# Kernel tuning notes

Measured on AMD Instinct MI355X. Metric: run time of the kernel, lower is better.

The kernel has to match this reference:

```python
import jax, jax.numpy as jnp
import numpy as np
from jax import lax

B, NR, NT, M, NUM_ITER = 16384, 64, 32, 4, 64


def setup_inputs() -> dict:
    key = jax.random.key(0)
    k1, k2, k3 = jax.random.split(key, 3)
    yt = jax.random.normal(k1, (B, NR), dtype=jnp.float32)
    # scale channel to keep the 64-step unrolled descent numerically stable
    Ht = 0.1 * jax.random.normal(k2, (B, NR, NT), dtype=jnp.float32)
    sigmat0 = 0.5 + 0.5 * jax.random.uniform(k3, (B,), dtype=jnp.float32)
    m = jnp.array([-3.0, -1.0, 1.0, 3.0], dtype=jnp.float32)          # 4-PAM constellation
    alpha = jnp.full((M,), 0.25, dtype=jnp.float32)                    # uniform prior
    taui = jnp.ones((NUM_ITER + 1,), dtype=jnp.float32)                # taui0 = 1
    delta = jnp.full((NUM_ITER,), 0.1, dtype=jnp.float32)              # delta0 = 0.1
    return {"yt": yt, "Ht": Ht, "sigmat0": sigmat0, "m": m, "alpha": alpha,
            "taui": taui, "delta": delta}


def reference(yt, Ht, sigmat0, m, alpha, taui, delta):
    # Precompute as in CMDNet.call
    HH = jnp.einsum('bri,brj->bij', Ht, Ht)          # [B, Nt, Nt] = H^T H
    yH = jnp.einsum('br,brj->bj', yt, Ht)            # [B, Nt]     = y^T H
    Bsz, _, Nt = Ht.shape
    Mc = m.shape[0]
    n_iter = delta.shape[0]

    G0 = jnp.zeros((Bsz, Nt, Mc), dtype=Ht.dtype)
    sig2 = (sigmat0 ** 2)[:, None, None]             # [B,1,1]
    log_alpha = jnp.log(alpha)                       # [M]
    taui_abs = jnp.abs(taui)                         # [num_iter+1]
    # first layer uses scale 1 in the softmax (first_iter=True), but taui_abs in grad_x
    ft_scale = taui_abs[:n_iter].at[0].set(1.0)

    def step(G, inp):
        scale, ta, d = inp
        ft = jax.nn.softmax((log_alpha + G) * scale, axis=-1)   # [B,Nt,M]
        xt = jnp.sum(ft * m, axis=-1)                           # [B,Nt] soft symbol
        xHH = jnp.einsum('bi,bij->bj', xt, HH)                  # [B,Nt]
        grad_x = ta * (ft * m - ft * xt[..., None])             # [B,Nt,M]
        grad_L = sig2 * (1.0 - jnp.exp(-G)) + grad_x * (xHH - yH)[..., None]
        return G - d * grad_L, None

    G, _ = lax.scan(step, G0, (ft_scale, taui_abs[:n_iter], delta))

    # last layer (last_iter=True): softmax + soft symbol only, no update
    ft = jax.nn.softmax((log_alpha + G) * taui_abs[n_iter], axis=-1)
    xt = jnp.sum(ft * m, axis=-1)
    return ft, xt
```

## Files before the change

kernel.cpp:

```cpp
#include <hip/hip_runtime.h>


#define NRr 64
#define NTt 32
#define NITER 64
#define B_TOTAL 16384

using f16x8  = __attribute__((ext_vector_type(8))) _Float16;
using h16x2  = __attribute__((ext_vector_type(2))) _Float16;
using f32x16 = __attribute__((ext_vector_type(16))) float;

static __device__ __forceinline__ uint32_t pk16(float a, float b) {
    union { _Float16 h[2]; uint32_t u; } x;
    x.h[0] = (_Float16)a; x.h[1] = (_Float16)b;
    return x.u;
}

static __device__ __forceinline__ float fdot2u(uint32_t a, uint32_t b, float c) {
    union { uint32_t u; h16x2 h; } x, y;
    x.u = a; y.u = b;
#if __has_builtin(__builtin_amdgcn_fdot2)
    return __builtin_amdgcn_fdot2(x.h, y.h, c, false);
#else
    return c + (float)x.h[0] * (float)y.h[0] + (float)x.h[1] * (float)y.h[1];
#endif
}

static __device__ __forceinline__ float exp2fast(float x) {
#if __has_builtin(__builtin_amdgcn_exp2f)
    return __builtin_amdgcn_exp2f(x);
#else
    return exp2f(x);
#endif
}

static __device__ __forceinline__ float rdlane(float v, int lane) {
    return __builtin_bit_cast(float,
        __builtin_amdgcn_readlane(__builtin_bit_cast(int, v), lane));
}

static __device__ __forceinline__ float rfl(float v) {
    return __builtin_bit_cast(float,
        __builtin_amdgcn_readfirstlane(__builtin_bit_cast(int, v)));
}

static __device__ __forceinline__ void gram_one(
    const float* __restrict__ hp, const float* __restrict__ ypt,
    const int hi, uint32_t ap[8], float& ypart_out)
{
    f32x16 acc = {};
    float  ypart = 0.f;
#pragma unroll
    for (int kc = 0; kc < 4; ++kc) {
        const int kb = kc * 16 + hi * 8;
        float h[8];
#pragma unroll
        for (int e = 0; e < 8; ++e) h[e] = hp[(size_t)(kb + e) * NTt];
        const float4 ya = *(const float4*)(ypt + kb);
        const float4 yb = *(const float4*)(ypt + kb + 4);
        ypart += h[0]*ya.x + h[1]*ya.y + h[2]*ya.z + h[3]*ya.w
               + h[4]*yb.x + h[5]*yb.y + h[6]*yb.z + h[7]*yb.w;
        f16x8 fa;
#pragma unroll
        for (int e = 0; e < 8; ++e) fa[e] = (_Float16)h[e];
        acc = __builtin_amdgcn_mfma_f32_32x32x16_f16(fa, fa, acc, 0, 0, 0);
    }
#pragma unroll
    for (int g = 0; g < 4; ++g) {
        ap[2*g+0] = pk16(acc[4*g+0], acc[4*g+1]);
        ap[2*g+1] = pk16(acc[4*g+2], acc[4*g+3]);
    }
    ypart_out = ypart;
}

static __device__ __forceinline__ void exch_hh(
    const uint32_t apx[8], const uint32_t apy[8], const int hi, uint32_t hh[16])
{
#pragma unroll
    for (int p = 0; p < 8; ++p) {
        const uint32_t snd = hi ? apx[p] : apy[p];
        const uint32_t rcv = (uint32_t)__shfl_xor((int)snd, 32, 64);
        const uint32_t own = hi ? apy[p] : apx[p];
        const int g = p >> 1, cc = p & 1;
        hh[4*g + cc]     = hi ? rcv : own;
        hh[4*g + 2 + cc] = hi ? own : rcv;
    }
}

__global__ __launch_bounds__(256)
__attribute__((amdgpu_waves_per_eu(4, 4)))
void cmdnet_kernel(
    const float* __restrict__ yt,
    const float* __restrict__ Ht,
    const float* __restrict__ sig0,
    const float* __restrict__ mm,
    const float* __restrict__ alpha,
    const float* __restrict__ taui,
    const float* __restrict__ delta,
    float* __restrict__ out)
{
    __shared__ __align__(16) _Float16 xtsh[4][4][32];

    const int tid = threadIdx.x;
    const int w   = tid >> 6;
    const int l   = tid & 63;
    const int j   = l & 31;
    const int hi  = l >> 5;
    const int c0  = (blockIdx.x * 4 + w) * 4;

    const float vta = fabsf(taui[l]);
    const float vd  = delta[l];

    const size_t hstride = (size_t)NRr * NTt;

    uint32_t hhA[16], hhB[16];
    float yHA_v, yHB_v;
    {
        uint32_t apx[8], apy[8];
        float ypx, ypy;
        gram_one(Ht + (size_t)(c0    ) * hstride + j, yt + (size_t)(c0    ) * NRr, hi, apx, ypx);
        gram_one(Ht + (size_t)(c0 + 2) * hstride + j, yt + (size_t)(c0 + 2) * NRr, hi, apy, ypy);
        exch_hh(apx, apy, hi, hhA);
        const float snd = hi ? ypx : ypy;
        const float rcv = __shfl_xor(snd, 32, 64);
        yHA_v = (hi ? ypy : ypx) + rcv;
    }
    {
        uint32_t apx[8], apy[8];
        float ypx, ypy;
        gram_one(Ht + (size_t)(c0 + 1) * hstride + j, yt + (size_t)(c0 + 1) * NRr, hi, apx, ypx);
        gram_one(Ht + (size_t)(c0 + 3) * hstride + j, yt + (size_t)(c0 + 3) * NRr, hi, apy, ypy);
        exch_hh(apx, apy, hi, hhB);
        const float snd = hi ? ypx : ypy;
        const float rcv = __shfl_xor(snd, 32, 64);
        yHB_v = (hi ? ypy : ypx) + rcv;
    }

    const int bA = c0 + 2*hi;
    const int bB = bA + 1;
    const float sgA = sig0[bA], sgB = sig0[bB];
    const float sig2A = sgA * sgA, sig2B = sgB * sgB;

    const float4 mv = *(const float4*)mm;
    const float4 av = *(const float4*)alpha;
    const float m0 = rfl(mv.x), m1 = rfl(mv.y), m2 = rfl(mv.z), m3 = rfl(mv.w);
    const float la0 = rfl(__log2f(av.x)), la1 = rfl(__log2f(av.y));
    const float la2 = rfl(__log2f(av.z)), la3 = rfl(__log2f(av.w));

    const float L2E  = 1.4426950408889634f;
    const float NL2E = -1.4426950408889634f;

    _Float16* xwA = &xtsh[w][2*hi][j];
    _Float16* xwB = &xtsh[w][2*hi+1][j];
    const uint4* xr = (const uint4*)&xtsh[w][2*hi][0];

    float GA0 = 0.f, GA1 = 0.f, GA2 = 0.f, GA3 = 0.f;
    float GB0 = 0.f, GB1 = 0.f, GB2 = 0.f, GB3 = 0.f;

#pragma unroll 2
    for (int it = 0; it < NITER; ++it) {
        const float ta  = rdlane(vta, it);
        const float d   = rdlane(vd,  it);
        const float sc  = (it == 0) ? 1.0f : ta;
        const float scL = sc * L2E;
        const float tad = ta * d;
        const float c1A = d * sig2A, c1B = d * sig2B;
        const float ls0 = la0 * sc, ls1 = la1 * sc,
                    ls2 = la2 * sc, ls3 = la3 * sc;

        const float sA0 = fmaf(GA0, scL, ls0), sA1 = fmaf(GA1, scL, ls1);
        const float sA2 = fmaf(GA2, scL, ls2), sA3 = fmaf(GA3, scL, ls3);
        const float sB0 = fmaf(GB0, scL, ls0), sB1 = fmaf(GB1, scL, ls1);
        const float sB2 = fmaf(GB2, scL, ls2), sB3 = fmaf(GB3, scL, ls3);
        const float mxA = fmaxf(fmaxf(fmaxf(sA0, sA1), sA2), sA3);
        const float mxB = fmaxf(fmaxf(fmaxf(sB0, sB1), sB2), sB3);
        const float eA0 = exp2fast(sA0 - mxA), eA1 = exp2fast(sA1 - mxA);
        const float eA2 = exp2fast(sA2 - mxA), eA3 = exp2fast(sA3 - mxA);
        const float eB0 = exp2fast(sB0 - mxB), eB1 = exp2fast(sB1 - mxB);
        const float eB2 = exp2fast(sB2 - mxB), eB3 = exp2fast(sB3 - mxB);
        const float ZA = (eA0 + eA1) + (eA2 + eA3);
        const float ZB = (eB0 + eB1) + (eB2 + eB3);
        const float RA = __builtin_amdgcn_rcpf(ZA);
        const float RB = __builtin_amdgcn_rcpf(ZB);
        const float SA = fmaf(eA0, m0, fmaf(eA1, m1, fmaf(eA2, m2, eA3 * m3)));
        const float SB = fmaf(eB0, m0, fmaf(eB1, m1, fmaf(eB2, m2, eB3 * m3)));
        const float xtA = SA * RA;
        const float xtB = SB * RB;

        *xwA = (_Float16)xtA;
        *xwB = (_Float16)xtB;
        asm volatile("" ::: "memory");

        const float enA0 = exp2fast(GA0 * NL2E), enA1 = exp2fast(GA1 * NL2E);
        const float enA2 = exp2fast(GA2 * NL2E), enA3 = exp2fast(GA3 * NL2E);
        const float enB0 = exp2fast(GB0 * NL2E), enB1 = exp2fast(GB1 * NL2E);
        const float enB2 = exp2fast(GB2 * NL2E), enB3 = exp2fast(GB3 * NL2E);

        float pA0 = 0.f, pA1 = 0.f, pB0 = 0.f, pB1 = 0.f;
        {
            const uint4 a0 = xr[0], a1 = xr[1];
            const uint4 b0 = xr[4], b1 = xr[5];
            pA0 = fdot2u(hhA[ 0], a0.x, pA0); pA1 = fdot2u(hhA[ 1], a0.y, pA1);
            pB0 = fdot2u(hhB[ 0], b0.x, pB0); pB1 = fdot2u(hhB[ 1], b0.y, pB1);
            pA0 = fdot2u(hhA[ 2], a0.z, pA0); pA1 = fdot2u(hhA[ 3], a0.w, pA1);
            pB0 = fdot2u(hhB[ 2], b0.z, pB0); pB1 = fdot2u(hhB[ 3], b0.w, pB1);
            pA0 = fdot2u(hhA[ 4], a1.x, pA0); pA1 = fdot2u(hhA[ 5], a1.y, pA1);
            pB0 = fdot2u(hhB[ 4], b1.x, pB0); pB1 = fdot2u(hhB[ 5], b1.y, pB1);
            pA0 = fdot2u(hhA[ 6], a1.z, pA0); pA1 = fdot2u(hhA[ 7], a1.w, pA1);
            pB0 = fdot2u(hhB[ 6], b1.z, pB0); pB1 = fdot2u(hhB[ 7], b1.w, pB1);
        }
        {
            const uint4 a2 = xr[2], a3 = xr[3];
            const uint4 b2 = xr[6], b3 = xr[7];
            pA0 = fdot2u(hhA[ 8], a2.x, pA0); pA1 = fdot2u(hhA[ 9], a2.y, pA1);
            pB0 = fdot2u(hhB[ 8], b2.x, pB0); pB1 = fdot2u(hhB[ 9], b2.y, pB1);
            pA0 = fdot2u(hhA[10], a2.z, pA0); pA1 = fdot2u(hhA[11], a2.w, pA1);
            pB0 = fdot2u(hhB[10], b2.z, pB0); pB1 = fdot2u(hhB[11], b2.w, pB1);
            pA0 = fdot2u(hhA[12], a3.x, pA0); pA1 = fdot2u(hhA[13], a3.y, pA1);
            pB0 = fdot2u(hhB[12], b3.x, pB0); pB1 = fdot2u(hhB[13], b3.y, pB1);
            pA0 = fdot2u(hhA[14], a3.z, pA0); pA1 = fdot2u(hhA[15], a3.w, pA1);
            pB0 = fdot2u(hhB[14], b3.z, pB0); pB1 = fdot2u(hhB[15], b3.w, pB1);
        }
        asm volatile("" ::: "memory");

        const float qdA = (pA0 + pA1) - yHA_v;
        const float qdB = (pB0 + pB1) - yHB_v;
        const float tqA = tad * qdA * RA;
        const float tqB = tad * qdB * RB;

        GA0 = fmaf(-tqA, eA0 * (m0 - xtA), fmaf(c1A, enA0, GA0 - c1A));
        GA1 = fmaf(-tqA, eA1 * (m1 - xtA), fmaf(c1A, enA1, GA1 - c1A));
        GA2 = fmaf(-tqA, eA2 * (m2 - xtA), fmaf(c1A, enA2, GA2 - c1A));
        GA3 = fmaf(-tqA, eA3 * (m3 - xtA), fmaf(c1A, enA3, GA3 - c1A));
        GB0 = fmaf(-tqB, eB0 * (m0 - xtB), fmaf(c1B, enB0, GB0 - c1B));
        GB1 = fmaf(-tqB, eB1 * (m1 - xtB), fmaf(c1B, enB1, GB1 - c1B));
        GB2 = fmaf(-tqB, eB2 * (m2 - xtB), fmaf(c1B, enB2, GB2 - c1B));
        GB3 = fmaf(-tqB, eB3 * (m3 - xtB), fmaf(c1B, enB3, GB3 - c1B));
    }

    const float tap = fabsf(taui[NITER]);
#pragma unroll
    for (int s = 0; s < 2; ++s) {
        const float G0 = s ? GB0 : GA0, G1 = s ? GB1 : GA1;
        const float G2 = s ? GB2 : GA2, G3 = s ? GB3 : GA3;
        const int   bm = s ? bB : bA;
        const float w0 = fmaf(G0, L2E, la0) * tap;
        const float w1 = fmaf(G1, L2E, la1) * tap;
        const float w2 = fmaf(G2, L2E, la2) * tap;
        const float w3 = fmaf(G3, L2E, la3) * tap;
        const float mx = fmaxf(fmaxf(fmaxf(w0, w1), w2), w3);
        const float e0 = exp2fast(w0 - mx), e1 = exp2fast(w1 - mx);
        const float e2 = exp2fast(w2 - mx), e3 = exp2fast(w3 - mx);
        const float Z  = (e0 + e1) + (e2 + e3);
        const float R  = __builtin_amdgcn_rcpf(Z);
        const float f0 = e0 * R, f1 = e1 * R, f2 = e2 * R, f3 = e3 * R;
        const float xt = fmaf(f0, m0, fmaf(f1, m1, fmaf(f2, m2, f3 * m3)));

        float4 f4; f4.x = f0; f4.y = f1; f4.z = f2; f4.w = f3;
        *(float4*)(out + ((size_t)bm * NTt + j) * 4) = f4;
        out[(size_t)B_TOTAL * NTt * 4 + (size_t)bm * NTt + j] = xt;
    }
}

extern "C" void kernel_launch(void* const* d_in, const int* in_sizes, int n_in,
                              void* d_out, int out_size, void* d_ws, size_t ws_size,
                              hipStream_t stream) {
    const float* yt    = (const float*)d_in[0];
    const float* Ht    = (const float*)d_in[1];
    const float* sig0  = (const float*)d_in[2];
    const float* mm    = (const float*)d_in[3];
    const float* alpha = (const float*)d_in[4];
    const float* taui  = (const float*)d_in[5];
    const float* delta = (const float*)d_in[6];
    float* out = (float*)d_out;

    const int blocks = B_TOTAL / 16;
    cmdnet_kernel<<<blocks, 256, 0, stream>>>(yt, Ht, sig0, mm, alpha, taui,
                                              delta, out);
}
```

Before: 94.46 us.

## Split Gram precompute and descent into two kernels via workspace

Splits the fused kernel in two. The first kernel computes H^T H (packed fp16) and y^T H into the workspace. The second kernel runs the 64-step descent with one batch per half-wave instead of two, which lowers register pressure and allows higher occupancy (waves_per_eu 6-8). The cost is an extra launch plus a round-trip of about 33 MB through global memory. The fused path is kept as a fallback when the workspace is too small.

```diff
diff --git a/kernel.cpp b/kernel.cpp
--- a/kernel.cpp
+++ b/kernel.cpp
@@ -5,6 +5,11 @@
 #define NTt 32
 #define NITER 64
 #define B_TOTAL 16384
+
+#define HH_WS_BYTES ((size_t)B_TOTAL * 512 * 4)
+#define YH_WS_OFF   HH_WS_BYTES
+#define YH_WS_BYTES ((size_t)B_TOTAL * NTt * 4)
+#define WS_NEEDED   (HH_WS_BYTES + YH_WS_BYTES)
 
 using f16x8  = __attribute__((ext_vector_type(8))) _Float16;
 using h16x2  = __attribute__((ext_vector_type(2))) _Float16;
@@ -88,16 +93,163 @@
 }
 
 __global__ __launch_bounds__(256)
+__attribute__((amdgpu_waves_per_eu(6, 8)))
+void cmdnet_gram(
+    const float* __restrict__ yt, const float* __restrict__ Ht,
+    uint4* __restrict__ wsHH, float* __restrict__ wsYH)
+{
+    const int tid = threadIdx.x;
+    const int w   = tid >> 6;
+    const int l   = tid & 63;
+    const int j   = l & 31;
+    const int hi  = l >> 5;
+    const int c0  = (blockIdx.x * 4 + w) * 2;
+
+    const size_t hstride = (size_t)NRr * NTt;
+
+    uint32_t apx[8], apy[8];
+    float ypx, ypy;
+    gram_one(Ht + (size_t)(c0    ) * hstride + j, yt + (size_t)(c0    ) * NRr, hi, apx, ypx);
+    gram_one(Ht + (size_t)(c0 + 1) * hstride + j, yt + (size_t)(c0 + 1) * NRr, hi, apy, ypy);
+
+    uint32_t hh[16];
+    exch_hh(apx, apy, hi, hh);
+    const float snd = hi ? ypx : ypy;
+    const float rcv = __shfl_xor(snd, 32, 64);
+    const float yH_v = (hi ? ypy : ypx) + rcv;
+
+    const int bmy = c0 + hi;
+#pragma unroll
+    for (int qg = 0; qg < 4; ++qg) {
+        uint4 v; v.x = hh[4*qg+0]; v.y = hh[4*qg+1];
+                 v.z = hh[4*qg+2]; v.w = hh[4*qg+3];
+        wsHH[(size_t)bmy * 128 + qg * 32 + j] = v;
+    }
+    wsYH[(size_t)bmy * NTt + j] = yH_v;
+}
+
+__global__ __launch_bounds__(256)
+__attribute__((amdgpu_waves_per_eu(6, 8)))
+void cmdnet_descent(
+    const uint4* __restrict__ wsHH, const float* __restrict__ wsYH,
+    const float* __restrict__ sig0, const float* __restrict__ mm,
+    const float* __restrict__ alpha, const float* __restrict__ taui,
+    const float* __restrict__ delta, float* __restrict__ out)
+{
+    __shared__ __align__(16) _Float16 xtsh[4][2][32];
+
+    const int tid = threadIdx.x;
+    const int w   = tid >> 6;
+    const int l   = tid & 63;
+    const int j   = l & 31;
+    const int hi  = l >> 5;
+    const int c0  = (blockIdx.x * 4 + w) * 2;
+    const int bmy = c0 + hi;
+
+    const float vta = fabsf(taui[l]);
+    const float vd  = delta[l];
+
+    uint32_t hh[16];
+#pragma unroll
+    for (int qg = 0; qg < 4; ++qg) {
+        const uint4 v = wsHH[(size_t)bmy * 128 + qg * 32 + j];
+        hh[4*qg+0] = v.x; hh[4*qg+1] = v.y; hh[4*qg+2] = v.z; hh[4*qg+3] = v.w;
+    }
+    const float yH_v = wsYH[(size_t)bmy * NTt + j];
+
+    const float sgv  = sig0[bmy];
+    const float sig2 = sgv * sgv;
+
+    const float4 mv = *(const float4*)mm;
+    const float4 av = *(const float4*)alpha;
+    const float m0 = rfl(mv.x), m1 = rfl(mv.y), m2 = rfl(mv.z), m3 = rfl(mv.w);
+    const float la0 = rfl(__log2f(av.x)), la1 = rfl(__log2f(av.y));
+    const float la2 = rfl(__log2f(av.z)), la3 = rfl(__log2f(av.w));
+
+    const float L2E  = 1.4426950408889634f;
+    const float NL2E = -1.4426950408889634f;
+
+    _Float16*    xwp = &xtsh[w][hi][j];
+    const uint4* xrp = (const uint4*)&xtsh[w][hi][0];
+
+    float G0 = 0.f, G1 = 0.f, G2 = 0.f, G3 = 0.f;
+
+    for (int it = 0; it < NITER; ++it) {
+        const float ta  = rdlane(vta, it);
+        const float d   = rdlane(vd,  it);
+        const float sc  = (it == 0) ? 1.0f : ta;
+        const float scL = sc * L2E;
+        const float tad = ta * d;
+        const float c1  = d * sig2;
+        const float ls0 = la0 * sc, ls1 = la1 * sc,
+                    ls2 = la2 * sc, ls3 = la3 * sc;
+
+        const float s0 = fmaf(G0, scL, ls0), s1 = fmaf(G1, scL, ls1);
+        const float s2 = fmaf(G2, scL, ls2), s3 = fmaf(G3, scL, ls3);
+        const float mx = fmaxf(fmaxf(fmaxf(s0, s1), s2), s3);
+        const float e0 = exp2fast(s0 - mx), e1 = exp2fast(s1 - mx);
+        const float e2 = exp2fast(s2 - mx), e3 = exp2fast(s3 - mx);
+        const float Z  = (e0 + e1) + (e2 + e3);
+        const float R  = __builtin_amdgcn_rcpf(Z);
+        const float S  = fmaf(e0, m0, fmaf(e1, m1, fmaf(e2, m2, e3 * m3)));
+        const float xt = S * R;
+
+        *xwp = (_Float16)xt;
+        asm volatile("" ::: "memory");
+
+        const float en0 = exp2fast(G0 * NL2E), en1 = exp2fast(G1 * NL2E);
+        const float en2 = exp2fast(G2 * NL2E), en3 = exp2fast(G3 * NL2E);
+
+        const uint4 a0 = xrp[0], a1 = xrp[1], a2 = xrp[2], a3 = xrp[3];
+        asm volatile("" ::: "memory");
+
+        float p0 = fdot2u(hh[ 0], a0.x, -yH_v);
+        float p1 = fdot2u(hh[ 1], a0.y, 0.f);
+        float p2 = fdot2u(hh[ 2], a0.z, 0.f);
+        float p3 = fdot2u(hh[ 3], a0.w, 0.f);
+        p0 = fdot2u(hh[ 4], a1.x, p0); p1 = fdot2u(hh[ 5], a1.y, p1);
+        p2 = fdot2u(hh[ 6], a1.z, p2); p3 = fdot2u(hh[ 7], a1.w, p3);
+        p0 = fdot2u(hh[ 8], a2.x, p0); p1 = fdot2u(hh[ 9], a2.y, p1);
+        p2 = fdot2u(hh[10], a2.z, p2); p3 = fdot2u(hh[11], a2.w, p3);
+        p0 = fdot2u(hh[12], a3.x, p0); p1 = fdot2u(hh[13], a3.y, p1);
+        p2 = fdot2u(hh[14], a3.z, p2); p3 = fdot2u(hh[15], a3.w, p3);
+
+        const float qd = (p0 + p1) + (p2 + p3);
+        const float tq = tad * qd * R;
+
+        G0 = fmaf(-tq, e0 * (m0 - xt), fmaf(c1, en0, G0 - c1));
+        G1 = fmaf(-tq, e1 * (m1 - xt), fmaf(c1, en1, G1 - c1));
+        G2 = fmaf(-tq, e2 * (m2 - xt), fmaf(c1, en2, G2 - c1));
+        G3 = fmaf(-tq, e3 * (m3 - xt), fmaf(c1, en3, G3 - c1));
+    }
+
+    const float tap = fabsf(taui[NITER]);
+    {
+        const float w0 = fmaf(G0, L2E, la0) * tap;
+        const float w1 = fmaf(G1, L2E, la1) * tap;
+        const float w2 = fmaf(G2, L2E, la2) * tap;
+        const float w3 = fmaf(G3, L2E, la3) * tap;
+        const float mx = fmaxf(fmaxf(fmaxf(w0, w1), w2), w3);
+        const float e0 = exp2fast(w0 - mx), e1 = exp2fast(w1 - mx);
+        const float e2 = exp2fast(w2 - mx), e3 = exp2fast(w3 - mx);
+        const float Z  = (e0 + e1) + (e2 + e3);
+        const float R  = __builtin_amdgcn_rcpf(Z);
+        const float f0 = e0 * R, f1 = e1 * R, f2 = e2 * R, f3 = e3 * R;
+        const float xt = fmaf(f0, m0, fmaf(f1, m1, fmaf(f2, m2, f3 * m3)));
+
+        float4 f4; f4.x = f0; f4.y = f1; f4.z = f2; f4.w = f3;
+        *(float4*)(out + ((size_t)bmy * NTt + j) * 4) = f4;
+        out[(size_t)B_TOTAL * NTt * 4 + (size_t)bmy * NTt + j] = xt;
+    }
+}
+
+__global__ __launch_bounds__(256)
 __attribute__((amdgpu_waves_per_eu(4, 4)))
-void cmdnet_kernel(
-    const float* __restrict__ yt,
-    const float* __restrict__ Ht,
-    const float* __restrict__ sig0,
-    const float* __restrict__ mm,
-    const float* __restrict__ alpha,
-    const float* __restrict__ taui,
-    const float* __restrict__ delta,
-    float* __restrict__ out)
+void cmdnet_mono(
+    const float* __restrict__ yt, const float* __restrict__ Ht,
+    const float* __restrict__ sig0, const float* __restrict__ mm,
+    const float* __restrict__ alpha, const float* __restrict__ taui,
+    const float* __restrict__ delta, float* __restrict__ out)
 {
     __shared__ __align__(16) _Float16 xtsh[4][4][32];
 
@@ -110,14 +262,12 @@
 
     const float vta = fabsf(taui[l]);
     const float vd  = delta[l];
-
     const size_t hstride = (size_t)NRr * NTt;
 
     uint32_t hhA[16], hhB[16];
     float yHA_v, yHB_v;
     {
-        uint32_t apx[8], apy[8];
-        float ypx, ypy;
+        uint32_t apx[8], apy[8]; float ypx, ypy;
         gram_one(Ht + (size_t)(c0    ) * hstride + j, yt + (size_t)(c0    ) * NRr, hi, apx, ypx);
         gram_one(Ht + (size_t)(c0 + 2) * hstride + j, yt + (size_t)(c0 + 2) * NRr, hi, apy, ypy);
         exch_hh(apx, apy, hi, hhA);
@@ -126,8 +276,7 @@
         yHA_v = (hi ? ypy : ypx) + rcv;
     }
     {
-        uint32_t apx[8], apy[8];
-        float ypx, ypy;
+        uint32_t apx[8], apy[8]; float ypx, ypy;
         gram_one(Ht + (size_t)(c0 + 1) * hstride + j, yt + (size_t)(c0 + 1) * NRr, hi, apx, ypx);
         gram_one(Ht + (size_t)(c0 + 3) * hstride + j, yt + (size_t)(c0 + 3) * NRr, hi, apy, ypy);
         exch_hh(apx, apy, hi, hhB);
@@ -274,7 +423,14 @@
     const float* delta = (const float*)d_in[6];
     float* out = (float*)d_out;
 
-    const int blocks = B_TOTAL / 16;
-    cmdnet_kernel<<<blocks, 256, 0, stream>>>(yt, Ht, sig0, mm, alpha, taui,
-                                              delta, out);
-}
+    if (ws_size >= WS_NEEDED && d_ws != nullptr) {
+        uint4* wsHH = (uint4*)d_ws;
+        float* wsYH = (float*)((char*)d_ws + YH_WS_OFF);
+        cmdnet_gram<<<B_TOTAL / 8, 256, 0, stream>>>(yt, Ht, wsHH, wsYH);
+        cmdnet_descent<<<B_TOTAL / 8, 256, 0, stream>>>(wsHH, wsYH, sig0, mm,
+                                                        alpha, taui, delta, out);
+    } else {
+        cmdnet_mono<<<B_TOTAL / 16, 256, 0, stream>>>(yt, Ht, sig0, mm, alpha,
+                                                      taui, delta, out);
+    }
+}
```

New measurement: 113.5 us. 1.2x slower.
